# Kernel optimization log

Hardware: AMD Instinct MI355X
Metric: run time of the kernel (lower is better)

## Reference

```python
import jax, jax.numpy as jnp
import numpy as np

B, C, P, N_PARTS, JOINTS_PER_PART = 2048, 256, 15, 5, 3
GROUPS = 4
EPS = 1e-5
MASK_VAL = 10000.0


def setup_inputs() -> dict:
    key = jax.random.key(0)
    k1, k2, k3 = jax.random.split(key, 3)
    g = (2 * C) // GROUPS  # 128
    return {
        "x": jax.random.normal(k1, (B, C, P, 1), jnp.float32),
        "conv_w": jax.random.normal(k2, (GROUPS, g, g), jnp.float32) * 0.05,
        "conv_b": jax.random.normal(k3, (2 * C,), jnp.float32) * 0.05,
        "bn_gamma": jnp.ones((2 * C,), jnp.float32),
        "bn_beta": jnp.zeros((2 * C,), jnp.float32),
    }


def reference(x, conv_w, conv_b, bn_gamma, bn_beta):
    Bb, Cc, Pp, _ = x.shape
    xs = x[..., 0]  # [B, C, P]

    # relative[b,c,i,k] = xs[b,c,k] - xs[b,c,i]; for a row i in part p the
    # reduction is max_k(relative - MASK_VAL * [k in part p]). Since the mask
    # only depends on the part of row i, precompute the per-part masked max of
    # xs over k and broadcast-subtract xs[i].
    part_id = jnp.arange(Pp) // JOINTS_PER_PART  # [P]
    Mg = jnp.where(part_id[None, :] == jnp.arange(N_PARTS)[:, None], -MASK_VAL, 0.0)  # [5, P]
    m = jnp.max(xs[:, :, None, :] + Mg[None, None, :, :], axis=-1)  # [B, C, 5]
    tmp = m[:, :, part_id] - xs  # [B, C, P]

    y = jnp.concatenate([xs, tmp], axis=1)  # [B, 2C, P]

    # grouped 1x1 conv (groups=4)
    g = (2 * Cc) // GROUPS
    y4 = y.reshape(Bb, GROUPS, g, Pp)
    z = jnp.einsum('bgip,goi->bgop', y4, conv_w).reshape(Bb, 2 * Cc, Pp)
    z = z + conv_b[None, :, None]

    # BatchNorm2d, training mode: biased batch stats over (B, spatial)
    mean = jnp.mean(z, axis=(0, 2))
    var = jnp.var(z, axis=(0, 2))
    zn = (z - mean[None, :, None]) * jax.lax.rsqrt(var + EPS)[None, :, None]
    out = jax.nn.relu(zn * bn_gamma[None, :, None] + bn_beta[None, :, None])
    return out[..., None]  # [B, 2C, P, 1]
```

## Files before the change

### kernel.cpp

```cpp
#include <hip/hip_runtime.h>
#include <hip/hip_bf16.h>
#include <cstdint>

#define EPS_ 1e-5f
#define NVALID_F 30720.0f

typedef __bf16 bf16x8 __attribute__((ext_vector_type(8)));
typedef float f32x16 __attribute__((ext_vector_type(16)));
typedef unsigned short u16x8 __attribute__((ext_vector_type(8)));
typedef float f32x4a4 __attribute__((ext_vector_type(4), aligned(4)));
typedef float f32x2a4 __attribute__((ext_vector_type(2), aligned(4)));

__device__ __forceinline__ unsigned short f2bf(float f) {
  unsigned u = __float_as_uint(f);
  u += 0x7FFFu + ((u >> 16) & 1u);
  return (unsigned short)(u >> 16);
}
__device__ __forceinline__ float bf2f(unsigned short h) {
  return __uint_as_float((unsigned)h << 16);
}

__global__ void k_wprep(const float* __restrict__ w, unsigned short* __restrict__ wf) {
  int q = blockIdx.x * 256 + threadIdx.x;
  int l = q & 63, ks = (q >> 6) & 7, mt = (q >> 9) & 3, g = q >> 11;
  int o = mt * 32 + (l & 31);
  int i = ks * 16 + (l >> 5) * 8;
  const float* src = w + ((size_t)(g * 128 + o) * 128 + i);
  u16x8 v;
#pragma unroll
  for (int j = 0; j < 8; ++j) v[j] = f2bf(src[j]);
  *(u16x8*)(wf + (size_t)q * 8) = v;
}

__global__ __launch_bounds__(256, 3) void k_gemm(const float* __restrict__ x,
                                                 const unsigned short* __restrict__ wf,
                                                 unsigned short* __restrict__ Z2,
                                                 float2* __restrict__ Part) {
  __shared__ unsigned short Yt[32 * 520];
  const int t = threadIdx.x;
  const int b0 = blockIdx.x * 2;

#pragma unroll
  for (int bi = 0; bi < 2; ++bi) {
    const float* xb = x + (size_t)(b0 + bi) * 3840 + t * 15;
    f32x4a4 u0 = *(const f32x4a4*)(xb);
    f32x4a4 u1 = *(const f32x4a4*)(xb + 4);
    f32x4a4 u2 = *(const f32x4a4*)(xb + 8);
    f32x2a4 u3 = *(const f32x2a4*)(xb + 12);
    float u4 = xb[14];
    float v[15];
#pragma unroll
    for (int j = 0; j < 4; ++j) { v[j] = u0[j]; v[4 + j] = u1[j]; v[8 + j] = u2[j]; }
    v[12] = u3[0]; v[13] = u3[1]; v[14] = u4;
    float pm[5];
#pragma unroll
    for (int q = 0; q < 5; ++q) pm[q] = fmaxf(fmaxf(v[3 * q], v[3 * q + 1]), v[3 * q + 2]);
    float mq[5];
    mq[0] = fmaxf(fmaxf(pm[1], pm[2]), fmaxf(pm[3], pm[4]));
    mq[1] = fmaxf(fmaxf(pm[0], pm[2]), fmaxf(pm[3], pm[4]));
    mq[2] = fmaxf(fmaxf(pm[0], pm[1]), fmaxf(pm[3], pm[4]));
    mq[3] = fmaxf(fmaxf(pm[0], pm[1]), fmaxf(pm[2], pm[4]));
    mq[4] = fmaxf(fmaxf(pm[0], pm[1]), fmaxf(pm[2], pm[3]));
    const int c0 = bi * 16;
#pragma unroll
    for (int p = 0; p < 15; ++p) {
      Yt[(c0 + p) * 520 + t] = f2bf(v[p]);
      Yt[(c0 + p) * 520 + 256 + t] = f2bf(mq[p / 3] - v[p]);
    }
    Yt[(c0 + 15) * 520 + t] = 0;
    Yt[(c0 + 15) * 520 + 256 + t] = 0;
  }
  __syncthreads();

  const int lane = t & 63, g = t >> 6;
  const int l31 = lane & 31, lh = lane >> 5;
  const bf16x8* Wfv = (const bf16x8*)wf;

  bf16x8 bfr[8];
  const unsigned short* yrow = &Yt[l31 * 520 + g * 128 + lh * 8];
#pragma unroll
  for (int ks = 0; ks < 8; ++ks)
    bfr[ks] = *(const bf16x8*)(yrow + ks * 16);

  bf16x8 wrA[8], wrB[8];
#pragma unroll
  for (int ks = 0; ks < 8; ++ks)
    wrA[ks] = Wfv[(size_t)((g * 4 + 0) * 8 + ks) * 64 + lane];

#define MT_STEP(MT, CUR, NXT, PRE)                                              \
  do {                                                                          \
    if (PRE) {                                                                  \
      _Pragma("unroll") for (int ks = 0; ks < 8; ++ks)                          \
          NXT[ks] = Wfv[(size_t)((g * 4 + (MT) + 1) * 8 + ks) * 64 + lane];     \
    }                                                                           \
    f32x16 acc;                                                                 \
    _Pragma("unroll") for (int r = 0; r < 16; ++r) acc[r] = 0.f;                \
    _Pragma("unroll") for (int ks = 0; ks < 8; ++ks)                            \
        acc = __builtin_amdgcn_mfma_f32_32x32x16_bf16(bfr[ks], CUR[ks], acc, 0, 0, 0); \
    float s = 0.f, s2 = 0.f;                                                    \
    _Pragma("unroll") for (int r = 0; r < 16; ++r) {                            \
      float vv = acc[r]; s += vv; s2 = fmaf(vv, vv, s2);                        \
    }                                                                           \
    s += __shfl_xor(s, 32, 64);                                                 \
    s2 += __shfl_xor(s2, 32, 64);                                               \
    const int ch = g * 128 + (MT) * 32 + l31;                                   \
    if (lane < 32) Part[(size_t)blockIdx.x * 512 + ch] = make_float2(s, s2);    \
    _Pragma("unroll") for (int r = 0; r < 16; ++r) {                            \
      int row = (r & 3) + 8 * (r >> 2) + 4 * lh;                                \
      int p = row & 15, bl = row >> 4;                                          \
      if (p != 15)                                                              \
        Z2[((size_t)(b0 + bl) * 15 + p) * 512 + ch] = f2bf(acc[r]);             \
    }                                                                           \
  } while (0)

  MT_STEP(0, wrA, wrB, 1);
  MT_STEP(1, wrB, wrA, 1);
  MT_STEP(2, wrA, wrB, 1);
  MT_STEP(3, wrB, wrA, 0);
#undef MT_STEP
}

__global__ void k_stats(const float2* __restrict__ Part,
                        const float* __restrict__ gamma, const float* __restrict__ beta,
                        float2* __restrict__ AB) {
  const int ch = blockIdx.x, t = threadIdx.x;
  float s = 0.f, s2 = 0.f;
#pragma unroll
  for (int i = 0; i < 4; ++i) {
    float2 v = Part[(size_t)(t + 256 * i) * 512 + ch];
    s += v.x; s2 += v.y;
  }
#pragma unroll
  for (int m = 32; m >= 1; m >>= 1) { s += __shfl_xor(s, m, 64); s2 += __shfl_xor(s2, m, 64); }
  __shared__ float ls[4], ls2[4];
  if ((t & 63) == 0) { ls[t >> 6] = s; ls2[t >> 6] = s2; }
  __syncthreads();
  if (t == 0) {
    float S = ls[0] + ls[1] + ls[2] + ls[3];
    float S2 = ls2[0] + ls2[1] + ls2[2] + ls2[3];
    const float inv = 1.f / NVALID_F;
    float mean = S * inv;
    float var = fmaxf(S2 * inv - mean * mean, 0.f);
    float a = gamma[ch] * rsqrtf(var + EPS_);
    AB[ch] = make_float2(a, beta[ch] - mean * a);
  }
}

__global__ __launch_bounds__(256, 3) void k_final(const unsigned short* __restrict__ Z2,
                                                  const float2* __restrict__ AB,
                                                  float* __restrict__ out) {
  __shared__ unsigned short zt[30 * 520];
  __shared__ float aArr[512], bArr[512];
  const int t = threadIdx.x;
  const int b0 = blockIdx.x * 2;

  const u16x8* src = (const u16x8*)(Z2 + (size_t)b0 * 15 * 512);
#pragma unroll
  for (int c = t; c < 1920; c += 256) {
    int row = c >> 6, off = (c & 63) * 8;
    *(u16x8*)&zt[row * 520 + off] = src[c];
  }
#pragma unroll
  for (int i = 0; i < 2; ++i) {
    int ch = i * 256 + t;
    float2 ab = AB[ch];
    aArr[ch] = ab.x; bArr[ch] = ab.y;
  }
  __syncthreads();

#pragma unroll
  for (int bi = 0; bi < 2; ++bi) {
    float2* slab = (float2*)(out + (size_t)(b0 + bi) * 7680);
#pragma unroll 5
    for (int k = 0; k < 15; ++k) {
      int e0 = k * 512 + 2 * t;
      int ch0 = e0 / 15, p0 = e0 - ch0 * 15;
      int e1 = e0 + 1;
      int ch1 = e1 / 15, p1 = e1 - ch1 * 15;
      float f0 = bf2f(zt[(bi * 15 + p0) * 520 + ch0]);
      float f1 = bf2f(zt[(bi * 15 + p1) * 520 + ch1]);
      slab[k * 256 + t] = make_float2(
          fmaxf(fmaf(f0, aArr[ch0], bArr[ch0]), 0.f),
          fmaxf(fmaf(f1, aArr[ch1], bArr[ch1]), 0.f));
    }
  }
}

extern "C" void kernel_launch(void* const* d_in, const int* in_sizes, int n_in,
                              void* d_out, int out_size, void* d_ws, size_t ws_size,
                              hipStream_t stream) {
  const float* x = (const float*)d_in[0];
  const float* cw = (const float*)d_in[1];
  const float* gamma = (const float*)d_in[3];
  const float* beta = (const float*)d_in[4];

  unsigned short* wf = (unsigned short*)d_ws;
  unsigned short* Z2 = wf + 65536;
  float2* Part = (float2*)(Z2 + (size_t)30720 * 512);
  float2* AB = Part + (size_t)1024 * 512;

  hipLaunchKernelGGL(k_wprep, dim3(32), dim3(256), 0, stream, cw, wf);
  hipLaunchKernelGGL(k_gemm, dim3(1024), dim3(256), 0, stream, x, wf, Z2, Part);
  hipLaunchKernelGGL(k_stats, dim3(512), dim3(256), 0, stream, Part, gamma, beta, AB);
  hipLaunchKernelGGL(k_final, dim3(1024), dim3(256), 0, stream, Z2, AB, (float*)d_out);
}
```

Before: 49.84 us.

## Recompute grouped conv in final pass instead of storing bf16 intermediate

Removes the bf16 Z2 intermediate buffer. The first pass now computes only the per-block BatchNorm partial sums. The final pass rebuilds Y from x, redoes the MFMA GEMM, and writes the result into shared memory before normalizing and writing the output. This trades a second read of x plus duplicated GEMM work for skipping the write and read-back of a roughly 31 MB intermediate.

```diff
diff --git a/kernel.cpp b/kernel.cpp
--- a/kernel.cpp
+++ b/kernel.cpp
@@ -32,14 +32,8 @@
   *(u16x8*)(wf + (size_t)q * 8) = v;
 }
 
-__global__ __launch_bounds__(256, 3) void k_gemm(const float* __restrict__ x,
-                                                 const unsigned short* __restrict__ wf,
-                                                 unsigned short* __restrict__ Z2,
-                                                 float2* __restrict__ Part) {
-  __shared__ unsigned short Yt[32 * 520];
-  const int t = threadIdx.x;
-  const int b0 = blockIdx.x * 2;
-
+__device__ __forceinline__ void build_Y(const float* __restrict__ x, int b0, int t,
+                                        unsigned short* __restrict__ Yt) {
 #pragma unroll
   for (int bi = 0; bi < 2; ++bi) {
     const float* xb = x + (size_t)(b0 + bi) * 3840 + t * 15;
@@ -70,6 +64,15 @@
     Yt[(c0 + 15) * 520 + t] = 0;
     Yt[(c0 + 15) * 520 + 256 + t] = 0;
   }
+}
+
+__global__ __launch_bounds__(256, 3) void k_pass1(const float* __restrict__ x,
+                                                  const unsigned short* __restrict__ wf,
+                                                  float2* __restrict__ Part) {
+  __shared__ unsigned short Yt[32 * 520];
+  const int t = threadIdx.x;
+  const int b0 = blockIdx.x * 2;
+  build_Y(x, b0, t, Yt);
   __syncthreads();
 
   const int lane = t & 63, g = t >> 6;
@@ -87,7 +90,7 @@
   for (int ks = 0; ks < 8; ++ks)
     wrA[ks] = Wfv[(size_t)((g * 4 + 0) * 8 + ks) * 64 + lane];
 
-#define MT_STEP(MT, CUR, NXT, PRE)                                              \
+#define MT_STEP1(MT, CUR, NXT, PRE)                                             \
   do {                                                                          \
     if (PRE) {                                                                  \
       _Pragma("unroll") for (int ks = 0; ks < 8; ++ks)                          \
@@ -105,19 +108,13 @@
     s2 += __shfl_xor(s2, 32, 64);                                               \
     const int ch = g * 128 + (MT) * 32 + l31;                                   \
     if (lane < 32) Part[(size_t)blockIdx.x * 512 + ch] = make_float2(s, s2);    \
-    _Pragma("unroll") for (int r = 0; r < 16; ++r) {                            \
-      int row = (r & 3) + 8 * (r >> 2) + 4 * lh;                                \
-      int p = row & 15, bl = row >> 4;                                          \
-      if (p != 15)                                                              \
-        Z2[((size_t)(b0 + bl) * 15 + p) * 512 + ch] = f2bf(acc[r]);             \
-    }                                                                           \
   } while (0)
 
-  MT_STEP(0, wrA, wrB, 1);
-  MT_STEP(1, wrB, wrA, 1);
-  MT_STEP(2, wrA, wrB, 1);
-  MT_STEP(3, wrB, wrA, 0);
-#undef MT_STEP
+  MT_STEP1(0, wrA, wrB, 1);
+  MT_STEP1(1, wrB, wrA, 1);
+  MT_STEP1(2, wrA, wrB, 1);
+  MT_STEP1(3, wrB, wrA, 0);
+#undef MT_STEP1
 }
 
 __global__ void k_stats(const float2* __restrict__ Part,
@@ -146,25 +143,61 @@
   }
 }
 
-__global__ __launch_bounds__(256, 3) void k_final(const unsigned short* __restrict__ Z2,
+__global__ __launch_bounds__(256, 3) void k_pass2(const float* __restrict__ x,
+                                                  const unsigned short* __restrict__ wf,
                                                   const float2* __restrict__ AB,
                                                   float* __restrict__ out) {
-  __shared__ unsigned short zt[30 * 520];
+  __shared__ unsigned short Yt[32 * 520];
   __shared__ float aArr[512], bArr[512];
   const int t = threadIdx.x;
   const int b0 = blockIdx.x * 2;
-
-  const u16x8* src = (const u16x8*)(Z2 + (size_t)b0 * 15 * 512);
-#pragma unroll
-  for (int c = t; c < 1920; c += 256) {
-    int row = c >> 6, off = (c & 63) * 8;
-    *(u16x8*)&zt[row * 520 + off] = src[c];
-  }
-#pragma unroll
-  for (int i = 0; i < 2; ++i) {
-    int ch = i * 256 + t;
-    float2 ab = AB[ch];
-    aArr[ch] = ab.x; bArr[ch] = ab.y;
+  build_Y(x, b0, t, Yt);
+  __syncthreads();
+
+  {
+    const int lane = t & 63, g = t >> 6;
+    const int l31 = lane & 31, lh = lane >> 5;
+    const bf16x8* Wfv = (const bf16x8*)wf;
+
+    bf16x8 bfr[8];
+    const unsigned short* yrow = &Yt[l31 * 520 + g * 128 + lh * 8];
+#pragma unroll
+    for (int ks = 0; ks < 8; ++ks)
+      bfr[ks] = *(const bf16x8*)(yrow + ks * 16);
+#pragma unroll
+    for (int i = 0; i < 2; ++i) {
+      int ch = i * 256 + t;
+      float2 ab = AB[ch];
+      aArr[ch] = ab.x; bArr[ch] = ab.y;
+    }
+
+    bf16x8 wrA[8], wrB[8];
+#pragma unroll
+    for (int ks = 0; ks < 8; ++ks)
+      wrA[ks] = Wfv[(size_t)((g * 4 + 0) * 8 + ks) * 64 + lane];
+
+#define MT_STEP2(MT, CUR, NXT, PRE)                                             \
+  do {                                                                          \
+    if (PRE) {                                                                  \
+      _Pragma("unroll") for (int ks = 0; ks < 8; ++ks)                          \
+          NXT[ks] = Wfv[(size_t)((g * 4 + (MT) + 1) * 8 + ks) * 64 + lane];     \
+    }                                                                           \
+    f32x16 acc;                                                                 \
+    _Pragma("unroll") for (int r = 0; r < 16; ++r) acc[r] = 0.f;                \
+    _Pragma("unroll") for (int ks = 0; ks < 8; ++ks)                            \
+        acc = __builtin_amdgcn_mfma_f32_32x32x16_bf16(bfr[ks], CUR[ks], acc, 0, 0, 0); \
+    const int ch = g * 128 + (MT) * 32 + l31;                                   \
+    _Pragma("unroll") for (int r = 0; r < 16; ++r) {                            \
+      int row = (r & 3) + 8 * (r >> 2) + 4 * lh;                                \
+      Yt[row * 520 + ch] = f2bf(acc[r]);      \
+    }                                                                           \
+  } while (0)
+
+    MT_STEP2(0, wrA, wrB, 1);
+    MT_STEP2(1, wrB, wrA, 1);
+    MT_STEP2(2, wrA, wrB, 1);
+    MT_STEP2(3, wrB, wrA, 0);
+#undef MT_STEP2
   }
   __syncthreads();
 
@@ -177,8 +210,8 @@
       int ch0 = e0 / 15, p0 = e0 - ch0 * 15;
       int e1 = e0 + 1;
       int ch1 = e1 / 15, p1 = e1 - ch1 * 15;
-      float f0 = bf2f(zt[(bi * 15 + p0) * 520 + ch0]);
-      float f1 = bf2f(zt[(bi * 15 + p1) * 520 + ch1]);
+      float f0 = bf2f(Yt[(bi * 16 + p0) * 520 + ch0]);
+      float f1 = bf2f(Yt[(bi * 16 + p1) * 520 + ch1]);
       slab[k * 256 + t] = make_float2(
           fmaxf(fmaf(f0, aArr[ch0], bArr[ch0]), 0.f),
           fmaxf(fmaf(f1, aArr[ch1], bArr[ch1]), 0.f));
@@ -195,12 +228,11 @@
   const float* beta = (const float*)d_in[4];
 
   unsigned short* wf = (unsigned short*)d_ws;
-  unsigned short* Z2 = wf + 65536;
-  float2* Part = (float2*)(Z2 + (size_t)30720 * 512);
+  float2* Part = (float2*)(wf + 65536);
   float2* AB = Part + (size_t)1024 * 512;
 
   hipLaunchKernelGGL(k_wprep, dim3(32), dim3(256), 0, stream, cw, wf);
-  hipLaunchKernelGGL(k_gemm, dim3(1024), dim3(256), 0, stream, x, wf, Z2, Part);
+  hipLaunchKernelGGL(k_pass1, dim3(1024), dim3(256), 0, stream, x, wf, Part);
   hipLaunchKernelGGL(k_stats, dim3(512), dim3(256), 0, stream, Part, gamma, beta, AB);
-  hipLaunchKernelGGL(k_final, dim3(1024), dim3(256), 0, stream, Z2, AB, (float*)d_out);
-}
+  hipLaunchKernelGGL(k_pass2, dim3(1024), dim3(256), 0, stream, x, wf, AB, (float*)d_out);
+}
```

Result: faster. 48.54 us (-2.6%).
